# Performance work log

Hardware: AMD Instinct MI355X
Metric: run time of the kernel (lower is better)

The kernel has to match this reference:

```python
import jax, jax.numpy as jnp
import numpy as np
from jax import lax

B, T, D, H = 64, 512, 256, 256


def lstm_scan(x_seq, Wih, Whh, bih, bhh):
    """Run an LSTMCell over time. x_seq: [B, T, D] -> hidden states [B, T, H].
    Gate order i, f, g, o (torch LSTMCell convention)."""
    Bv, Tv, _ = x_seq.shape
    Hv = Whh.shape[1]
    # Precompute input projection once: [B, T, 4H]
    x_proj = jnp.einsum('btd,gd->btg', x_seq, Wih) + bih + bhh

    def step(carry, xp):
        h, c = carry
        gates = xp + h @ Whh.T  # [B, 4H]
        i, f, g, o = jnp.split(gates, 4, axis=-1)
        c = jax.nn.sigmoid(f) * c + jax.nn.sigmoid(i) * jnp.tanh(g)
        h = jax.nn.sigmoid(o) * jnp.tanh(c)
        return (h, c), h

    init = (jnp.zeros((Bv, Hv), x_seq.dtype), jnp.zeros((Bv, Hv), x_seq.dtype))
    _, hs = lax.scan(step, init, jnp.swapaxes(x_proj, 0, 1))  # [T, B, H]
    return jnp.swapaxes(hs, 0, 1)


def bilstm(x, input_length, Wih_f, Whh_f, bih_f, bhh_f, Wih_b, Whh_b, bih_b, bhh_b):
    Bv, L, _ = x.shape
    t = jnp.arange(L)
    lens = input_length.astype(jnp.int32)
    # Inversed input exactly as _get_inversed_input: for t < len -> x[len-1-t],
    # for t >= len -> x[L-1-(t-len)] (unused tail, faithful to original).
    inv_idx = L - 1 - ((L - lens[:, None] + t[None, :]) % L)  # [B, L]
    xn = jnp.take_along_axis(x, inv_idx[:, :, None], axis=1)

    fwd_h = lstm_scan(x, Wih_f, Whh_f, bih_f, bhh_f)   # [B, L, H]
    bwd_h = lstm_scan(xn, Wih_b, Whh_b, bih_b, bhh_b)  # [B, L, H]

    # Re-reverse the backward states over valid region; zero-pad beyond length.
    mask = t[None, :] < lens[:, None]                   # [B, L]
    bwd_idx = jnp.clip(lens[:, None] - 1 - t[None, :], 0, L - 1)
    bwd_g = jnp.take_along_axis(bwd_h, bwd_idx[:, :, None], axis=1)
    out = jnp.concatenate([fwd_h, bwd_g], axis=-1)      # [B, L, 2H]
    return jnp.where(mask[:, :, None], out, jnp.zeros((), out.dtype))


def setup_inputs() -> dict:
    key = jax.random.key(0)
    ks = jax.random.split(key, 10)
    s = 0.05
    return {
        'x': jax.random.normal(ks[0], (B, T, D), jnp.float32),
        'input_length': jax.random.randint(ks[1], (B,), 1, T + 1, jnp.int32),
        'Wih_f': jax.random.normal(ks[2], (4 * H, D), jnp.float32) * s,
        'Whh_f': jax.random.normal(ks[3], (4 * H, H), jnp.float32) * s,
        'bih_f': jax.random.normal(ks[4], (4 * H,), jnp.float32) * s,
        'bhh_f': jax.random.normal(ks[5], (4 * H,), jnp.float32) * s,
        'Wih_b': jax.random.normal(ks[6], (4 * H, D), jnp.float32) * s,
        'Whh_b': jax.random.normal(ks[7], (4 * H, H), jnp.float32) * s,
        'bih_b': jax.random.normal(ks[8], (4 * H,), jnp.float32) * s,
        'bhh_b': jax.random.normal(ks[9], (4 * H,), jnp.float32) * s,
    }


def reference(x, input_length, Wih_f, Whh_f, bih_f, bhh_f, Wih_b, Whh_b, bih_b, bhh_b):
    return bilstm(x, input_length, Wih_f, Whh_f, bih_f, bhh_f, Wih_b, Whh_b, bih_b, bhh_b)
```

## Files before the change

kernel.cpp:

```cpp
#include <hip/hip_runtime.h>
#include <cstdio>


typedef unsigned short ushort_t;
typedef __attribute__((ext_vector_type(8))) short short8;
typedef __attribute__((ext_vector_type(4))) float f32x4;
typedef __attribute__((ext_vector_type(4))) int i32x4;

__device__ __forceinline__ ushort_t f2bf(float f) {
    union { float f; unsigned u; } v; v.f = f;
    unsigned r = v.u + 0x7fffu + ((v.u >> 16) & 1u);
    return (ushort_t)(r >> 16);
}
__device__ __forceinline__ float bf2f(ushort_t h) {
    union { unsigned u; float f; } v; v.u = ((unsigned)h) << 16;
    return v.f;
}

__device__ __forceinline__ float fexp2(float x) {
#if __has_builtin(__builtin_amdgcn_exp2f)
    return __builtin_amdgcn_exp2f(x);
#else
    return exp2f(x);
#endif
}
__device__ __forceinline__ float frcp(float x) {
#if __has_builtin(__builtin_amdgcn_rcpf)
    return __builtin_amdgcn_rcpf(x);
#else
    return 1.0f / x;
#endif
}
__device__ __forceinline__ float fsig(float x) {
    return frcp(1.0f + fexp2(-1.44269504089f * x));
}
__device__ __forceinline__ float ftanh(float x) {
    float e = fexp2(2.88539008178f * x);
    return 1.0f - 2.0f * frcp(e + 1.0f);
}

__device__ __forceinline__ void lds_barrier() {
    asm volatile("s_waitcnt lgkmcnt(0)\n\ts_barrier" ::: "memory");
}

__device__ __forceinline__ void async_load16(const void* g, void* l) {
    __builtin_amdgcn_global_load_lds(
        (const __attribute__((address_space(1))) void*)g,
        (__attribute__((address_space(3))) void*)l, 16, 0, 0);
}

__global__ __launch_bounds__(256) void k_f2bf(const float* __restrict__ in,
                                              ushort_t* __restrict__ out, int n) {
    int i = (blockIdx.x * 256 + threadIdx.x) * 4;
    if (i + 3 < n) {
        float4 v = *(const float4*)&in[i];
        ushort4 o;
        o.x = f2bf(v.x); o.y = f2bf(v.y); o.z = f2bf(v.z); o.w = f2bf(v.w);
        *(ushort4*)&out[i] = o;
    }
}

__global__ __launch_bounds__(256) void k_wih(const float* __restrict__ wihf,
                                             const float* __restrict__ wihb,
                                             ushort_t* __restrict__ dst) {
    int d = blockIdx.y;
    int n = blockIdx.x * 4 + (threadIdx.x >> 6);
    int l = threadIdx.x & 63;
    const float* src = (d ? wihb : wihf) + (size_t)n * 256;
    float4 v = *(const float4*)&src[l * 4];
    int np = (n & 255) * 4 + (n >> 8);
    ushort4 o;
    o.x = f2bf(v.x); o.y = f2bf(v.y); o.z = f2bf(v.z); o.w = f2bf(v.w);
    *(ushort4*)&dst[((size_t)d * 1024 + np) * 256 + l * 4] = o;
}

__global__ __launch_bounds__(256) void k_bias(const float* __restrict__ bihf,
                                              const float* __restrict__ bhhf,
                                              const float* __restrict__ bihb,
                                              const float* __restrict__ bhhb,
                                              float* __restrict__ bv) {
    int i = blockIdx.x * 256 + threadIdx.x;
    int d = i >> 10, n = i & 1023;
    float s = d ? (bihb[n] + bhhb[n]) : (bihf[n] + bhhf[n]);
    bv[d * 1024 + (n & 255) * 4 + (n >> 8)] = s;
}

__global__ __launch_bounds__(256) void k_quant(const float* __restrict__ whhf,
                                               const float* __restrict__ whhb,
                                               int* __restrict__ wmf,
                                               float* __restrict__ fscale4) {
    int rowg = blockIdx.x * 4 + (threadIdx.x >> 6);
    int l = threadIdx.x & 63;
    int d = rowg >> 10;
    int row = rowg & 1023;
    const float* W = (d ? whhb : whhf) + (size_t)row * 256;
    float4 v = *(const float4*)&W[l * 4];
    float m = fmaxf(fmaxf(fabsf(v.x), fabsf(v.y)), fmaxf(fabsf(v.z), fabsf(v.w)));
    #pragma unroll
    for (int off = 32; off > 0; off >>= 1) m = fmaxf(m, __shfl_xor(m, off));
    float inv = (m > 0.0f) ? (127.0f / m) : 0.0f;
    int q0 = __float2int_rn(v.x * inv);
    int q1 = __float2int_rn(v.y * inv);
    int q2 = __float2int_rn(v.z * inv);
    int q3 = __float2int_rn(v.w * inv);
    q0 = min(127, max(-127, q0)); q1 = min(127, max(-127, q1));
    q2 = min(127, max(-127, q2)); q3 = min(127, max(-127, q3));
    int packed = (q0 & 255) | ((q1 & 255) << 8) | ((q2 & 255) << 16) | ((q3 & 255) << 24);
    int j = row & 255, gate = row >> 8;
    int row_p = j * 4 + gate;
    int Mt = row_p >> 4, rl = row_p & 15;
    int Kt = l >> 4, lg = (l >> 2) & 3, dw = l & 3;
    wmf[d * 65536 + ((Mt * 4 + Kt) * 64 + lg * 16 + rl) * 4 + dw] = packed;
    if (l == 0) fscale4[d * 1024 + row_p] = m / (127.0f * 127.0f);
}

#define LDSOFF(r, kc) ((r) * 32 + ((((kc) + ((r) >> 1)) & 3) * 8))

__global__ __launch_bounds__(256) void k_gemm(const ushort_t* __restrict__ A,
                                              const ushort_t* __restrict__ Bw,
                                              const float* __restrict__ biasv,
                                              const int* __restrict__ lens,
                                              ushort_t* __restrict__ Xp) {
    const int dir = blockIdx.z;
    const int tn = blockIdx.x;
    const int tm = blockIdx.y;

    {
        int lenb = lens[tm >> 2];
        if (lenb > 512) lenb = 512;
        if ((tm & 3) * 128 >= lenb) return;
    }

    const ushort_t* Bmat = Bw + dir * 262144;
    const float* bv = biasv + dir * 1024;
    ushort_t* C = Xp + (size_t)dir * 33554432;
    const int tid = threadIdx.x;
    const int w = tid >> 6, l = tid & 63;
    const int wm = w & 1, wn = w >> 1;

    __shared__ ushort_t As[2][4096] __attribute__((aligned(16)));
    __shared__ ushort_t Bs[2][4096] __attribute__((aligned(16)));

    f32x4 acc[4][4];
    #pragma unroll
    for (int i = 0; i < 4; i++)
        #pragma unroll
        for (int jj = 0; jj < 4; jj++) acc[i][jj] = (f32x4){0.f, 0.f, 0.f, 0.f};

    const int r0 = tid >> 2, cb = tid & 3;
    const int cs = (cb - (r0 >> 1)) & 3;
    const ushort_t* Arow0 = &A[(size_t)(tm * 128 + r0) * 256 + cs * 8];
    const ushort_t* Arow1 = Arow0 + (size_t)64 * 256;
    const ushort_t* Brow0 = &Bmat[(size_t)(tn * 128 + r0) * 256 + cs * 8];
    const ushort_t* Brow1 = Brow0 + (size_t)64 * 256;
    const int lw = w * 512;

#define GISSUE(KB, CUR)                                   \
    async_load16(Arow0 + (KB) * 32, &As[CUR][lw]);        \
    async_load16(Arow1 + (KB) * 32, &As[CUR][2048 + lw]); \
    async_load16(Brow0 + (KB) * 32, &Bs[CUR][lw]);        \
    async_load16(Brow1 + (KB) * 32, &Bs[CUR][2048 + lw]);

#define GCOMPUTE(CUR)                                                         \
    {                                                                         \
        short8 af[4], bfr[4];                                                 \
        const int q = l >> 4;                                                 \
        _Pragma("unroll")                                                     \
        for (int mt = 0; mt < 4; mt++) {                                      \
            int rr = wm * 64 + mt * 16 + (l & 15);                            \
            af[mt] = *(const short8*)&As[CUR][LDSOFF(rr, q)];                 \
        }                                                                     \
        _Pragma("unroll")                                                     \
        for (int nt = 0; nt < 4; nt++) {                                      \
            int rr = wn * 64 + nt * 16 + (l & 15);                            \
            bfr[nt] = *(const short8*)&Bs[CUR][LDSOFF(rr, q)];                \
        }                                                                     \
        _Pragma("unroll")                                                     \
        for (int mt = 0; mt < 4; mt++)                                        \
            _Pragma("unroll")                                                 \
            for (int nt = 0; nt < 4; nt++)                                    \
                acc[mt][nt] = __builtin_amdgcn_mfma_f32_16x16x32_bf16(        \
                    af[mt], bfr[nt], acc[mt][nt], 0, 0, 0);                   \
    }

#define GSTEP(KB, CUR, VML, DOISSUE)                                          \
    asm volatile("s_waitcnt vmcnt(" VML ")\n\ts_barrier" ::: "memory");       \
    GCOMPUTE(CUR);                                                            \
    lds_barrier();                                                            \
    if (DOISSUE) { GISSUE((KB) + 2, CUR) }

    GISSUE(0, 0)
    GISSUE(1, 1)
    GSTEP(0, 0, "4", 1)
    GSTEP(1, 1, "4", 1)
    GSTEP(2, 0, "4", 1)
    GSTEP(3, 1, "4", 1)
    GSTEP(4, 0, "4", 1)
    GSTEP(5, 1, "4", 1)
    GSTEP(6, 0, "4", 0)
    GSTEP(7, 1, "0", 0)
#undef GSTEP
#undef GCOMPUTE
#undef GISSUE

    #pragma unroll
    for (int nt = 0; nt < 4; nt++) {
        int n = tn * 128 + wn * 64 + nt * 16 + (l & 15);
        float bn = bv[n];
        #pragma unroll
        for (int mt = 0; mt < 4; mt++) {
            #pragma unroll
            for (int rr = 0; rr < 4; rr++) {
                int m = tm * 128 + wm * 64 + mt * 16 + (l >> 4) * 4 + rr;
                C[(size_t)m * 1024 + n] = f2bf(acc[mt][nt][rr] + bn);
            }
        }
    }
}

__global__ __launch_bounds__(512, 2) void k_rec(const ushort_t* __restrict__ xproj,
                                                const int* __restrict__ wmf,
                                                const float* __restrict__ fscale4,
                                                const int* __restrict__ lens,
                                                float* __restrict__ out) {
    const int b = blockIdx.x, d = blockIdx.y;
    const int tid = threadIdx.x;
    const int w = tid >> 6, l = tid & 63;
    int len = lens[b];
    if (len < 1) len = 1;
    if (len > 512) len = 512;
    const int lenm1 = len - 1;
    const bool dneg = (d != 0);
    const ushort_t* xp = xproj + ((size_t)d * 64 + b) * 524288;

    const int rg = l >> 4;
    const int rg16 = rg * 16;
    const int til = l & 7;
    const bool act = (l & 15) < 8;
    const int j = (w * 8 + til) * 4 + rg;

    i32x4 wf[8][4];
    const int* wb = wmf + d * 65536;
    #pragma unroll
    for (int i = 0; i < 8; i++)
        #pragma unroll
        for (int kt = 0; kt < 4; kt++)
            wf[i][kt] = *(const i32x4*)&wb[(((w * 8 + i) * 4 + kt) * 64 + l) * 4];
    #pragma unroll
    for (int i = 0; i < 8; i++)
        #pragma unroll
        for (int kt = 0; kt < 4; kt++)
            asm volatile("" : "+v"(wf[i][kt]));

    float4 fr = *(const float4*)&fscale4[d * 1024 + 4 * j];

    __shared__ char h8[2][256] __attribute__((aligned(16)));
    if (tid < 64) ((int*)h8)[tid] = 0;

    {
        float4 z = {0.f, 0.f, 0.f, 0.f};
        int total4 = (512 - len) * 64;
        for (int i = tid; i < total4; i += 512) {
            int t = len + (i >> 6);
            int c4 = i & 63;
            *(float4*)&out[((size_t)b * 512 + t) * 512 + d * 256 + c4 * 4] = z;
        }
    }
    __syncthreads();

    float c_state = 0.0f;
    const i32x4 z4 = {0, 0, 0, 0};
    const char* const xpl = (const char*)(xp + 4 * j);
    char* const outl = (char*)(out + (size_t)b * 262144 + d * 256 + j);

    uint2 xe = *(const uint2*)(xpl + (size_t)(dneg ? lenm1 : 0) * 2048);
    uint2 xo;
    {
        int sc = (1 < lenm1) ? 1 : lenm1;
        xo = *(const uint2*)(xpl + (size_t)(dneg ? (lenm1 - sc) : sc) * 2048);
    }

#define REC_STEP(RB, WB, XREG, S)                                              \
    do {                                                                       \
        const char* hbp = (const char*)h8[RB];                                 \
        i32x4 h0 = *(const i32x4*)(hbp + rg16);                                \
        i32x4 h1 = *(const i32x4*)(hbp + 64 + rg16);                           \
        i32x4 h2 = *(const i32x4*)(hbp + 128 + rg16);                          \
        i32x4 h3 = *(const i32x4*)(hbp + 192 + rg16);                          \
        uint2 xc = XREG;                                                       \
        {                                                                      \
            int sc2 = (S) + 2; if (sc2 > lenm1) sc2 = lenm1;                   \
            int t2 = dneg ? (lenm1 - sc2) : sc2;                               \
            XREG = *(const uint2*)(xpl + (size_t)t2 * 2048);                   \
        }                                                                      \
        i32x4 acc[8];                                                          \
        _Pragma("unroll")                                                      \
        for (int i = 0; i < 8; i++)                                            \
            acc[i] = __builtin_amdgcn_mfma_i32_16x16x64_i8(wf[i][0], h0, z4, 0, 0, 0); \
        _Pragma("unroll")                                                      \
        for (int i = 0; i < 8; i++)                                            \
            acc[i] = __builtin_amdgcn_mfma_i32_16x16x64_i8(wf[i][1], h1, acc[i], 0, 0, 0); \
        _Pragma("unroll")                                                      \
        for (int i = 0; i < 8; i++)                                            \
            acc[i] = __builtin_amdgcn_mfma_i32_16x16x64_i8(wf[i][2], h2, acc[i], 0, 0, 0); \
        _Pragma("unroll")                                                      \
        for (int i = 0; i < 8; i++)                                            \
            acc[i] = __builtin_amdgcn_mfma_i32_16x16x64_i8(wf[i][3], h3, acc[i], 0, 0, 0); \
        if (act) {                                                             \
            i32x4 q0 = (til & 1) ? acc[1] : acc[0];                            \
            i32x4 q1 = (til & 1) ? acc[3] : acc[2];                            \
            i32x4 q2 = (til & 1) ? acc[5] : acc[4];                            \
            i32x4 q3 = (til & 1) ? acc[7] : acc[6];                            \
            i32x4 r0 = (til & 2) ? q1 : q0;                                    \
            i32x4 r1 = (til & 2) ? q3 : q2;                                    \
            i32x4 u  = (til & 4) ? r1 : r0;                                    \
            float pi = bf2f((ushort_t)(xc.x & 0xffffu)) + fr.x * (float)u.x;   \
            float pf = bf2f((ushort_t)(xc.x >> 16))     + fr.y * (float)u.y;   \
            float pg = bf2f((ushort_t)(xc.y & 0xffffu)) + fr.z * (float)u.z;   \
            float po = bf2f((ushort_t)(xc.y >> 16))     + fr.w * (float)u.w;   \
            float ig = fsig(pi), fg = fsig(pf), gg = ftanh(pg), og = fsig(po); \
            c_state = fg * c_state + ig * gg;                                  \
            float h = og * ftanh(c_state);                                     \
            int qq = __float2int_rn(h * 127.0f);                               \
            qq = min(127, max(-127, qq));                                      \
            h8[WB][j] = (char)qq;                                              \
            int t = dneg ? (lenm1 - (S)) : (S);                                \
            *(float*)(outl + (size_t)t * 2048) = h;                            \
        }                                                                      \
        lds_barrier();                                                         \
    } while (0)

    int s = 0;
    for (; s + 1 < len; s += 2) {
        REC_STEP(0, 1, xe, s);
        REC_STEP(1, 0, xo, s + 1);
    }
    if (len & 1) {
        REC_STEP(0, 1, xe, s);
    }
#undef REC_STEP
}

extern "C" void kernel_launch(void* const* d_in, const int* in_sizes, int n_in,
                              void* d_out, int out_size, void* d_ws, size_t ws_size,
                              hipStream_t stream) {
    (void)in_sizes; (void)n_in; (void)out_size;
    const float* x    = (const float*)d_in[0];
    const int*   lens = (const int*)d_in[1];
    const float* wihf = (const float*)d_in[2];
    const float* whhf = (const float*)d_in[3];
    const float* bihf = (const float*)d_in[4];
    const float* bhhf = (const float*)d_in[5];
    const float* wihb = (const float*)d_in[6];
    const float* whhb = (const float*)d_in[7];
    const float* bihb = (const float*)d_in[8];
    const float* bhhb = (const float*)d_in[9];
    float* out = (float*)d_out;

    char* ws = (char*)d_ws;
    ushort_t* xbf    = (ushort_t*)(ws + 0);
    ushort_t* wihbf  = (ushort_t*)(ws + 16777216);
    float*    biasv  = (float*)(ws + 17825792);
    int*      wmf    = (int*)(ws + 17833984);
    float*    fscale4= (float*)(ws + 18358272);
    ushort_t* xproj  = (ushort_t*)(ws + 18366464);
    const size_t REQ = 18366464 + 134217728ull;
    if (ws_size < REQ) {
        fprintf(stderr, "kernel_launch: ws too small: %zu < %zu\n", ws_size, REQ);
    }

    k_f2bf<<<8192, 256, 0, stream>>>(x, xbf, 8388608);
    k_wih<<<dim3(256, 2), 256, 0, stream>>>(wihf, wihb, wihbf);
    k_bias<<<8, 256, 0, stream>>>(bihf, bhhf, bihb, bhhb, biasv);
    k_quant<<<512, 256, 0, stream>>>(whhf, whhb, wmf, fscale4);
    k_gemm<<<dim3(8, 256, 2), 256, 0, stream>>>(xbf, wihbf, biasv, lens, xproj);
    k_rec<<<dim3(64, 2), 512, 0, stream>>>(xproj, wmf, fscale4, lens, out);
}
```

Baseline: 520.0 us.

## Fuse input-projection GEMM into recurrent kernel and merge prep kernels

The four small preprocessing kernels (x to bf16, Wih conversion, bias sum, Whh int8 quantisation) are merged into one launch that dispatches on block index. The separate input-projection GEMM kernel is removed. Each recurrent block (one per batch row and direction) now computes its own x·Wih projection for its valid timesteps, using 128x128 tiles and 8 waves, before starting the recurrence. This cuts launch count and inter-kernel gaps, but the GEMM now runs on only 128 blocks instead of a large grid, so it loses parallelism and may lengthen the critical path.

New measurement: 611.5 us. 1.18x slower.

```diff
diff --git a/kernel.cpp b/kernel.cpp
--- a/kernel.cpp
+++ b/kernel.cpp
@@ -49,121 +49,115 @@
         (__attribute__((address_space(3))) void*)l, 16, 0, 0);
 }
 
-__global__ __launch_bounds__(256) void k_f2bf(const float* __restrict__ in,
-                                              ushort_t* __restrict__ out, int n) {
-    int i = (blockIdx.x * 256 + threadIdx.x) * 4;
-    if (i + 3 < n) {
-        float4 v = *(const float4*)&in[i];
+__global__ __launch_bounds__(256) void k_prep(
+        const float* __restrict__ x, ushort_t* __restrict__ xbf,
+        const float* __restrict__ wihf, const float* __restrict__ wihb,
+        ushort_t* __restrict__ wihbf,
+        const float* __restrict__ bihf, const float* __restrict__ bhhf,
+        const float* __restrict__ bihb, const float* __restrict__ bhhb,
+        float* __restrict__ biasv,
+        const float* __restrict__ whhf, const float* __restrict__ whhb,
+        int* __restrict__ wmf, float* __restrict__ fscale4) {
+    const int bid = blockIdx.x;
+    const int tid = threadIdx.x;
+    if (bid < 8192) {
+        int i = (bid * 256 + tid) * 4;
+        float4 v = *(const float4*)&x[i];
         ushort4 o;
         o.x = f2bf(v.x); o.y = f2bf(v.y); o.z = f2bf(v.z); o.w = f2bf(v.w);
-        *(ushort4*)&out[i] = o;
-    }
-}
-
-__global__ __launch_bounds__(256) void k_wih(const float* __restrict__ wihf,
-                                             const float* __restrict__ wihb,
-                                             ushort_t* __restrict__ dst) {
-    int d = blockIdx.y;
-    int n = blockIdx.x * 4 + (threadIdx.x >> 6);
-    int l = threadIdx.x & 63;
-    const float* src = (d ? wihb : wihf) + (size_t)n * 256;
-    float4 v = *(const float4*)&src[l * 4];
-    int np = (n & 255) * 4 + (n >> 8);
-    ushort4 o;
-    o.x = f2bf(v.x); o.y = f2bf(v.y); o.z = f2bf(v.z); o.w = f2bf(v.w);
-    *(ushort4*)&dst[((size_t)d * 1024 + np) * 256 + l * 4] = o;
-}
-
-__global__ __launch_bounds__(256) void k_bias(const float* __restrict__ bihf,
-                                              const float* __restrict__ bhhf,
-                                              const float* __restrict__ bihb,
-                                              const float* __restrict__ bhhb,
-                                              float* __restrict__ bv) {
-    int i = blockIdx.x * 256 + threadIdx.x;
-    int d = i >> 10, n = i & 1023;
-    float s = d ? (bihb[n] + bhhb[n]) : (bihf[n] + bhhf[n]);
-    bv[d * 1024 + (n & 255) * 4 + (n >> 8)] = s;
-}
-
-__global__ __launch_bounds__(256) void k_quant(const float* __restrict__ whhf,
-                                               const float* __restrict__ whhb,
-                                               int* __restrict__ wmf,
-                                               float* __restrict__ fscale4) {
-    int rowg = blockIdx.x * 4 + (threadIdx.x >> 6);
-    int l = threadIdx.x & 63;
-    int d = rowg >> 10;
-    int row = rowg & 1023;
-    const float* W = (d ? whhb : whhf) + (size_t)row * 256;
-    float4 v = *(const float4*)&W[l * 4];
-    float m = fmaxf(fmaxf(fabsf(v.x), fabsf(v.y)), fmaxf(fabsf(v.z), fabsf(v.w)));
-    #pragma unroll
-    for (int off = 32; off > 0; off >>= 1) m = fmaxf(m, __shfl_xor(m, off));
-    float inv = (m > 0.0f) ? (127.0f / m) : 0.0f;
-    int q0 = __float2int_rn(v.x * inv);
-    int q1 = __float2int_rn(v.y * inv);
-    int q2 = __float2int_rn(v.z * inv);
-    int q3 = __float2int_rn(v.w * inv);
-    q0 = min(127, max(-127, q0)); q1 = min(127, max(-127, q1));
-    q2 = min(127, max(-127, q2)); q3 = min(127, max(-127, q3));
-    int packed = (q0 & 255) | ((q1 & 255) << 8) | ((q2 & 255) << 16) | ((q3 & 255) << 24);
-    int j = row & 255, gate = row >> 8;
-    int row_p = j * 4 + gate;
-    int Mt = row_p >> 4, rl = row_p & 15;
-    int Kt = l >> 4, lg = (l >> 2) & 3, dw = l & 3;
-    wmf[d * 65536 + ((Mt * 4 + Kt) * 64 + lg * 16 + rl) * 4 + dw] = packed;
-    if (l == 0) fscale4[d * 1024 + row_p] = m / (127.0f * 127.0f);
+        *(ushort4*)&xbf[i] = o;
+    } else if (bid < 8704) {
+        int local = bid - 8192;
+        int d = local >> 8;
+        int n = (local & 255) * 4 + (tid >> 6);
+        int l = tid & 63;
+        const float* src = (d ? wihb : wihf) + (size_t)n * 256;
+        float4 v = *(const float4*)&src[l * 4];
+        int np = (n & 255) * 4 + (n >> 8);
+        ushort4 o;
+        o.x = f2bf(v.x); o.y = f2bf(v.y); o.z = f2bf(v.z); o.w = f2bf(v.w);
+        *(ushort4*)&wihbf[((size_t)d * 1024 + np) * 256 + l * 4] = o;
+    } else if (bid < 8712) {
+        int i = (bid - 8704) * 256 + tid;
+        int d = i >> 10, n = i & 1023;
+        float s = d ? (bihb[n] + bhhb[n]) : (bihf[n] + bhhf[n]);
+        biasv[d * 1024 + (n & 255) * 4 + (n >> 8)] = s;
+    } else {
+        int rowg = (bid - 8712) * 4 + (tid >> 6);
+        int l = tid & 63;
+        int d = rowg >> 10;
+        int row = rowg & 1023;
+        const float* W = (d ? whhb : whhf) + (size_t)row * 256;
+        float4 v = *(const float4*)&W[l * 4];
+        float m = fmaxf(fmaxf(fabsf(v.x), fabsf(v.y)), fmaxf(fabsf(v.z), fabsf(v.w)));
+        #pragma unroll
+        for (int off = 32; off > 0; off >>= 1) m = fmaxf(m, __shfl_xor(m, off));
+        float inv = (m > 0.0f) ? (127.0f / m) : 0.0f;
+        int q0 = __float2int_rn(v.x * inv);
+        int q1 = __float2int_rn(v.y * inv);
+        int q2 = __float2int_rn(v.z * inv);
+        int q3 = __float2int_rn(v.w * inv);
+        q0 = min(127, max(-127, q0)); q1 = min(127, max(-127, q1));
+        q2 = min(127, max(-127, q2)); q3 = min(127, max(-127, q3));
+        int packed = (q0 & 255) | ((q1 & 255) << 8) | ((q2 & 255) << 16) | ((q3 & 255) << 24);
+        int j = row & 255, gate = row >> 8;
+        int row_p = j * 4 + gate;
+        int Mt = row_p >> 4, rl = row_p & 15;
+        int Kt = l >> 4, lg = (l >> 2) & 3, dw = l & 3;
+        wmf[d * 65536 + ((Mt * 4 + Kt) * 64 + lg * 16 + rl) * 4 + dw] = packed;
+        if (l == 0) fscale4[d * 1024 + row_p] = m / (127.0f * 127.0f);
+    }
 }
 
 #define LDSOFF(r, kc) ((r) * 32 + ((((kc) + ((r) >> 1)) & 3) * 8))
 
-__global__ __launch_bounds__(256) void k_gemm(const ushort_t* __restrict__ A,
-                                              const ushort_t* __restrict__ Bw,
-                                              const float* __restrict__ biasv,
-                                              const int* __restrict__ lens,
-                                              ushort_t* __restrict__ Xp) {
-    const int dir = blockIdx.z;
-    const int tn = blockIdx.x;
-    const int tm = blockIdx.y;
-
-    {
-        int lenb = lens[tm >> 2];
-        if (lenb > 512) lenb = 512;
-        if ((tm & 3) * 128 >= lenb) return;
-    }
-
-    const ushort_t* Bmat = Bw + dir * 262144;
-    const float* bv = biasv + dir * 1024;
-    ushort_t* C = Xp + (size_t)dir * 33554432;
+__global__ __launch_bounds__(512, 2) void k_rec(
+        const ushort_t* __restrict__ xbf, const ushort_t* __restrict__ wihbf,
+        const float* __restrict__ biasv,
+        const int* __restrict__ wmf, const float* __restrict__ fscale4,
+        const int* __restrict__ lens,
+        ushort_t* __restrict__ xproj, float* __restrict__ out) {
+    const int b = blockIdx.x, d = blockIdx.y;
     const int tid = threadIdx.x;
     const int w = tid >> 6, l = tid & 63;
-    const int wm = w & 1, wn = w >> 1;
+    int len = lens[b];
+    if (len < 1) len = 1;
+    if (len > 512) len = 512;
 
     __shared__ ushort_t As[2][4096] __attribute__((aligned(16)));
     __shared__ ushort_t Bs[2][4096] __attribute__((aligned(16)));
-
-    f32x4 acc[4][4];
-    #pragma unroll
-    for (int i = 0; i < 4; i++)
-        #pragma unroll
-        for (int jj = 0; jj < 4; jj++) acc[i][jj] = (f32x4){0.f, 0.f, 0.f, 0.f};
-
-    const int r0 = tid >> 2, cb = tid & 3;
-    const int cs = (cb - (r0 >> 1)) & 3;
-    const ushort_t* Arow0 = &A[(size_t)(tm * 128 + r0) * 256 + cs * 8];
-    const ushort_t* Arow1 = Arow0 + (size_t)64 * 256;
-    const ushort_t* Brow0 = &Bmat[(size_t)(tn * 128 + r0) * 256 + cs * 8];
-    const ushort_t* Brow1 = Brow0 + (size_t)64 * 256;
-    const int lw = w * 512;
-
-#define GISSUE(KB, CUR)                                   \
-    async_load16(Arow0 + (KB) * 32, &As[CUR][lw]);        \
-    async_load16(Arow1 + (KB) * 32, &As[CUR][2048 + lw]); \
-    async_load16(Brow0 + (KB) * 32, &Bs[CUR][lw]);        \
-    async_load16(Brow1 + (KB) * 32, &Bs[CUR][2048 + lw]);
-
-#define GCOMPUTE(CUR)                                                         \
+    __shared__ char h8[2][256] __attribute__((aligned(16)));
+
+    {
+        const ushort_t* Bmat = wihbf + d * 262144;
+        const float* bv = biasv + d * 1024;
+        ushort_t* Cb = xproj + (size_t)d * 33554432 + (size_t)b * 524288;
+        const int wm = w & 1, wn = w >> 1;
+
+        const int r0 = tid >> 2, cbk = tid & 3;
+        const int cs = (cbk - (r0 >> 1)) & 3;
+        const int lw = w * 512;
+
+        const int mcn = (len + 127) >> 7;
+        for (int mc = 0; mc < mcn; mc++) {
+            const ushort_t* Arow =
+                &xbf[((size_t)b * 512 + mc * 128 + r0) * 256 + cs * 8];
+            for (int nc = 0; nc < 8; nc++) {
+                const ushort_t* Brow = &Bmat[(size_t)(nc * 128 + r0) * 256 + cs * 8];
+                f32x4 acc[4][2];
+                #pragma unroll
+                for (int i = 0; i < 4; i++)
+                    #pragma unroll
+                    for (int jj = 0; jj < 2; jj++)
+                        acc[i][jj] = (f32x4){0.f, 0.f, 0.f, 0.f};
+
+#define GEMM_ISSUE(KB, CUR)                                   \
+    async_load16(Arow + (KB) * 32, &As[CUR][lw]);             \
+    async_load16(Brow + (KB) * 32, &Bs[CUR][lw]);
+
+#define GEMM_COMPUTE(CUR)                                                     \
     {                                                                         \
-        short8 af[4], bfr[4];                                                 \
+        short8 af[4], bfr[2];                                                 \
         const int q = l >> 4;                                                 \
         _Pragma("unroll")                                                     \
         for (int mt = 0; mt < 4; mt++) {                                      \
@@ -171,64 +165,57 @@
             af[mt] = *(const short8*)&As[CUR][LDSOFF(rr, q)];                 \
         }                                                                     \
         _Pragma("unroll")                                                     \
-        for (int nt = 0; nt < 4; nt++) {                                      \
-            int rr = wn * 64 + nt * 16 + (l & 15);                            \
+        for (int nt = 0; nt < 2; nt++) {                                      \
+            int rr = wn * 32 + nt * 16 + (l & 15);                            \
             bfr[nt] = *(const short8*)&Bs[CUR][LDSOFF(rr, q)];                \
         }                                                                     \
         _Pragma("unroll")                                                     \
         for (int mt = 0; mt < 4; mt++)                                        \
             _Pragma("unroll")                                                 \
-            for (int nt = 0; nt < 4; nt++)                                    \
+            for (int nt = 0; nt < 2; nt++)                                    \
                 acc[mt][nt] = __builtin_amdgcn_mfma_f32_16x16x32_bf16(        \
                     af[mt], bfr[nt], acc[mt][nt], 0, 0, 0);                   \
     }
 
-#define GSTEP(KB, CUR, VML, DOISSUE)                                          \
+#define GEMM_STEP(KB, CUR, VML, DOISSUE)                                      \
     asm volatile("s_waitcnt vmcnt(" VML ")\n\ts_barrier" ::: "memory");       \
-    GCOMPUTE(CUR);                                                            \
+    GEMM_COMPUTE(CUR);                                                        \
     lds_barrier();                                                            \
-    if (DOISSUE) { GISSUE((KB) + 2, CUR) }
-
-    GISSUE(0, 0)
-    GISSUE(1, 1)
-    GSTEP(0, 0, "4", 1)
-    GSTEP(1, 1, "4", 1)
-    GSTEP(2, 0, "4", 1)
-    GSTEP(3, 1, "4", 1)
-    GSTEP(4, 0, "4", 1)
-    GSTEP(5, 1, "4", 1)
-    GSTEP(6, 0, "4", 0)
-    GSTEP(7, 1, "0", 0)
-#undef GSTEP
-#undef GCOMPUTE
-#undef GISSUE
-
-    #pragma unroll
-    for (int nt = 0; nt < 4; nt++) {
-        int n = tn * 128 + wn * 64 + nt * 16 + (l & 15);
-        float bn = bv[n];
-        #pragma unroll
-        for (int mt = 0; mt < 4; mt++) {
-            #pragma unroll
-            for (int rr = 0; rr < 4; rr++) {
-                int m = tm * 128 + wm * 64 + mt * 16 + (l >> 4) * 4 + rr;
-                C[(size_t)m * 1024 + n] = f2bf(acc[mt][nt][rr] + bn);
+    if (DOISSUE) { GEMM_ISSUE((KB) + 2, CUR) }
+
+                GEMM_ISSUE(0, 0)
+                GEMM_ISSUE(1, 1)
+                GEMM_STEP(0, 0, "2", 1)
+                GEMM_STEP(1, 1, "2", 1)
+                GEMM_STEP(2, 0, "2", 1)
+                GEMM_STEP(3, 1, "2", 1)
+                GEMM_STEP(4, 0, "2", 1)
+                GEMM_STEP(5, 1, "2", 1)
+                GEMM_STEP(6, 0, "2", 0)
+                GEMM_STEP(7, 1, "0", 0)
+#undef GEMM_STEP
+#undef GEMM_COMPUTE
+#undef GEMM_ISSUE
+
+                #pragma unroll
+                for (int nt = 0; nt < 2; nt++) {
+                    int n = nc * 128 + wn * 32 + nt * 16 + (l & 15);
+                    float bn = bv[n];
+                    #pragma unroll
+                    for (int mt = 0; mt < 4; mt++) {
+                        #pragma unroll
+                        for (int rr = 0; rr < 4; rr++) {
+                            int m = mc * 128 + wm * 64 + mt * 16 + (l >> 4) * 4 + rr;
+                            Cb[(size_t)m * 1024 + n] = f2bf(acc[mt][nt][rr] + bn);
+                        }
+                    }
+                }
             }
         }
     }
-}
-
-__global__ __launch_bounds__(512, 2) void k_rec(const ushort_t* __restrict__ xproj,
-                                                const int* __restrict__ wmf,
-                                                const float* __restrict__ fscale4,
-                                                const int* __restrict__ lens,
-                                                float* __restrict__ out) {
-    const int b = blockIdx.x, d = blockIdx.y;
-    const int tid = threadIdx.x;
-    const int w = tid >> 6, l = tid & 63;
-    int len = lens[b];
-    if (len < 1) len = 1;
-    if (len > 512) len = 512;
+    asm volatile("s_waitcnt vmcnt(0)" ::: "memory");
+    __syncthreads();
+
     const int lenm1 = len - 1;
     const bool dneg = (d != 0);
     const ushort_t* xp = xproj + ((size_t)d * 64 + b) * 524288;
@@ -254,7 +241,6 @@
 
     float4 fr = *(const float4*)&fscale4[d * 1024 + 4 * j];
 
-    __shared__ char h8[2][256] __attribute__((aligned(16)));
     if (tid < 64) ((int*)h8)[tid] = 0;
 
     {
@@ -369,10 +355,9 @@
         fprintf(stderr, "kernel_launch: ws too small: %zu < %zu\n", ws_size, REQ);
     }
 
-    k_f2bf<<<8192, 256, 0, stream>>>(x, xbf, 8388608);
-    k_wih<<<dim3(256, 2), 256, 0, stream>>>(wihf, wihb, wihbf);
-    k_bias<<<8, 256, 0, stream>>>(bihf, bhhf, bihb, bhhb, biasv);
-    k_quant<<<512, 256, 0, stream>>>(whhf, whhb, wmf, fscale4);
-    k_gemm<<<dim3(8, 256, 2), 256, 0, stream>>>(xbf, wihbf, biasv, lens, xproj);
-    k_rec<<<dim3(64, 2), 512, 0, stream>>>(xproj, wmf, fscale4, lens, out);
-}
+    k_prep<<<9224, 256, 0, stream>>>(x, xbf, wihf, wihb, wihbf,
+                                     bihf, bhhf, bihb, bhhb, biasv,
+                                     whhf, whhb, wmf, fscale4);
+    k_rec<<<dim3(64, 2), 512, 0, stream>>>(xbf, wihbf, biasv, wmf, fscale4,
+                                           lens, xproj, out);
+}
```
